# Performance work log

Measured on AMD Instinct MI355X. Metric: run time of the kernel, lower is better.

The kernel has to match this reference:

```python
import jax, jax.numpy as jnp
import numpy as np

B, T, D = 4, 2048, 1024

def setup_inputs() -> dict:
    key = jax.random.key(0)
    kx, kq, kk, kv = jax.random.split(key, 4)
    lim = 1.0 / np.sqrt(D)
    x = jax.random.normal(kx, (B, T, D), dtype=jnp.float32)
    # nn.Linear weights (stored as [out,in]); applied as x @ W.T
    W_q = jax.random.uniform(kq, (D, D), jnp.float32, -lim, lim)
    W_k = jax.random.uniform(kk, (D, D), jnp.float32, -lim, lim)
    W_v = jax.random.uniform(kv, (D, D), jnp.float32, -lim, lim)
    return {"x": x, "W_q": W_q, "W_k": W_k, "W_v": W_v}

def reference(x, W_q, W_k, W_v):
    d = x.shape[-1]
    Q = jnp.einsum('btd,ed->bte', x, W_q)
    K = jnp.einsum('btd,ed->bte', x, W_k)
    V = jnp.einsum('btd,ed->bte', x, W_v)
    att = jnp.einsum('bqd,bkd->bqk', Q, K) / jnp.sqrt(jnp.asarray(d, x.dtype))
    weights = jax.nn.softmax(att, axis=-1)  # NOTE: original applies no causal mask
    return jnp.einsum('bqk,bkd->bqd', weights, V)
```

## Files before the change

kernel.cpp:

```cpp
#include <hip/hip_runtime.h>
#include <hip/hip_bf16.h>
#include <math.h>
#include <type_traits>


typedef short shortx8 __attribute__((ext_vector_type(8)));
typedef short shortx4 __attribute__((ext_vector_type(4)));
typedef float floatx16 __attribute__((ext_vector_type(16)));
typedef __attribute__((address_space(3))) void lds_void_t;
typedef __attribute__((address_space(1))) const void gmem_void_t;

#define GLD16(gp, lp) \
    __builtin_amdgcn_global_load_lds((gmem_void_t*)(gp), (lds_void_t*)(lp), 16, 0, 0)

#define MODE_PROJ 0
#define MODE_EXP  1
#define MODE_DIV  2

template <int MODE>
__global__ __launch_bounds__(256, 2) void mfma_gemm_abt(
    const __hip_bfloat16* __restrict__ A, const __hip_bfloat16* __restrict__ B,
    void* __restrict__ Cv, float* __restrict__ rowsum,
    __hip_bfloat16* __restrict__ Vt,
    int M, int N, int K, long sA, long sB, long sC, float alpha)
{
    __shared__ __hip_bfloat16 lds[2 * 12288];

    using CT = std::conditional_t<MODE == MODE_DIV, float, __hip_bfloat16>;

    const int z = blockIdx.z;
    A += (long)z * sA;
    B += (long)z * sB;
    CT* C = (CT*)Cv + (long)z * sC;

    const int t     = threadIdx.x;
    const int wave  = t >> 6;
    const int lane  = t & 63;
    const int m0    = blockIdx.x * 256;
    const int n0    = blockIdx.y * 128;
    const int wm    = (wave >> 1) * 128;
    const int wn    = (wave & 1) * 64;
    const int lrow  = lane & 31;
    const int lhalf = lane >> 5;

    const long KU   = (long)(K >> 4);
    const long aSrc = (long)((m0 >> 5) + 2 * wave) * KU * 512 + lane * 8;
    const long bSrc = (long)((n0 >> 5) + wave) * KU * 512 + lane * 8;
    const int  dA   = wave * 2048;
    const int  dB   = 8192 + wave * 1024;

    const int raB = (wave >> 1) * 4096 + lane * 8;
    const int rbB = 8192 + (wave & 1) * 2048 + lane * 8;

#define STAGE(bo_, kt_) do {                                                  \
        _Pragma("unroll")                                                     \
        for (int q = 0; q < 2; ++q) {                                         \
            GLD16(A + aSrc + (long)(2 * (kt_) + q) * 512,                     \
                  lds + (bo_) + dA + q * 512);                                \
            GLD16(A + aSrc + (KU + 2 * (kt_) + q) * 512,                      \
                  lds + (bo_) + dA + 1024 + q * 512);                         \
            GLD16(B + bSrc + (long)(2 * (kt_) + q) * 512,                     \
                  lds + (bo_) + dB + q * 512);                                \
        }                                                                     \
    } while (0)

    floatx16 acc[4][2] = {};
    const int KT = K >> 5;

    STAGE(0, 0);
    asm volatile("s_waitcnt vmcnt(0)" ::: "memory");
    __builtin_amdgcn_s_barrier();

    for (int kt = 0; kt < KT; ++kt) {
        if (kt + 1 < KT)
            STAGE(((kt + 1) & 1) * 12288, kt + 1);

        const __hip_bfloat16* Ls = lds + (kt & 1) * 12288;

        #pragma unroll
        for (int s = 0; s < 2; ++s) {
            shortx8 a[4], b[2];
            #pragma unroll
            for (int i = 0; i < 4; ++i)
                a[i] = *(const shortx8*)(Ls + raB + i * 1024 + s * 512);
            #pragma unroll
            for (int j = 0; j < 2; ++j)
                b[j] = *(const shortx8*)(Ls + rbB + j * 1024 + s * 512);
            __builtin_amdgcn_s_setprio(1);
            #pragma unroll
            for (int i = 0; i < 4; ++i)
                #pragma unroll
                for (int j = 0; j < 2; ++j)
                    acc[i][j] = __builtin_amdgcn_mfma_f32_32x32x16_bf16(
                        a[i], b[j], acc[i][j], 0, 0, 0);
            __builtin_amdgcn_s_setprio(0);
        }
        asm volatile("s_waitcnt vmcnt(0)" ::: "memory");
        __builtin_amdgcn_s_barrier();
    }
#undef STAGE

    auto sidx = [&](int row, int col) -> long {
        return ((long)(row >> 5) * (N >> 4) + (col >> 4)) * 512
             + ((row & 31) + 32 * ((col >> 3) & 1)) * 8 + (col & 7);
    };

    if constexpr (MODE == MODE_PROJ) {
        if (z == 2) {
            const int bz   = m0 >> 11;
            const long bo2 = (long)bz * N * 2048;
            #pragma unroll
            for (int i = 0; i < 4; ++i)
                #pragma unroll
                for (int j = 0; j < 2; ++j)
                    #pragma unroll
                    for (int g = 0; g < 4; ++g) {
                        const int t0 = (m0 + wm + 32 * i + g * 8 + 4 * lhalf) & 2047;
                        const int d  = n0 + wn + 32 * j + lrow;
                        shortx4 pk;
                        #pragma unroll
                        for (int r = 0; r < 4; ++r) {
                            __hip_bfloat16 hb = __float2bfloat16(acc[i][j][4 * g + r]);
                            pk[r] = *(short*)&hb;
                        }
                        const long idx = bo2
                            + ((long)(d >> 5) * 128 + (t0 >> 4)) * 512
                            + ((d & 31) + 32 * ((t0 >> 3) & 1)) * 8 + (t0 & 7);
                        *(shortx4*)(Vt + idx) = pk;
                    }
        } else {
            #pragma unroll
            for (int i = 0; i < 4; ++i)
                #pragma unroll
                for (int j = 0; j < 2; ++j)
                    #pragma unroll
                    for (int g = 0; g < 4; ++g)
                        #pragma unroll
                        for (int r = 0; r < 4; ++r) {
                            const int row = m0 + wm + 32 * i + g * 8 + 4 * lhalf + r;
                            const int col = n0 + wn + 32 * j + lrow;
                            C[sidx(row, col)] = __float2bfloat16(acc[i][j][4 * g + r]);
                        }
        }
    } else if constexpr (MODE == MODE_EXP) {
        #pragma unroll
        for (int i = 0; i < 4; ++i) {
            float rs[16];
            #pragma unroll
            for (int reg = 0; reg < 16; ++reg) rs[reg] = 0.0f;
            #pragma unroll
            for (int j = 0; j < 2; ++j)
                #pragma unroll
                for (int g = 0; g < 4; ++g)
                    #pragma unroll
                    for (int r = 0; r < 4; ++r) {
                        const int row = m0 + wm + 32 * i + g * 8 + 4 * lhalf + r;
                        const int col = n0 + wn + 32 * j + lrow;
                        const float e = __expf(acc[i][j][4 * g + r] * alpha);
                        rs[4 * g + r] += e;
                        C[sidx(row, col)] = __float2bfloat16(e);
                    }
            #pragma unroll
            for (int reg = 0; reg < 16; ++reg) {
                float v = rs[reg];
                v += __shfl_xor(v, 1);
                v += __shfl_xor(v, 2);
                v += __shfl_xor(v, 4);
                v += __shfl_xor(v, 8);
                v += __shfl_xor(v, 16);
                if (lrow == 0) {
                    const long row = m0 + wm + 32 * i + (reg >> 2) * 8 + 4 * lhalf + (reg & 3);
                    atomicAdd(&rowsum[(long)z * M + row], v);
                }
            }
        }
    } else {
        #pragma unroll
        for (int i = 0; i < 4; ++i) {
            float inv[16];
            #pragma unroll
            for (int g = 0; g < 4; ++g)
                #pragma unroll
                for (int r = 0; r < 4; ++r) {
                    const long row = m0 + wm + 32 * i + g * 8 + 4 * lhalf + r;
                    inv[4 * g + r] = 1.0f / rowsum[(long)z * M + row];
                }
            #pragma unroll
            for (int j = 0; j < 2; ++j)
                #pragma unroll
                for (int g = 0; g < 4; ++g)
                    #pragma unroll
                    for (int r = 0; r < 4; ++r) {
                        const long row = m0 + wm + 32 * i + g * 8 + 4 * lhalf + r;
                        const long col = n0 + wn + 32 * j + lrow;
                        C[row * N + col] = acc[i][j][4 * g + r] * inv[4 * g + r];
                    }
        }
    }
}

__global__ __launch_bounds__(256) void prep(
    const float* __restrict__ x,
    const float* __restrict__ W0, const float* __restrict__ W1,
    const float* __restrict__ W2,
    __hip_bfloat16* __restrict__ xb, __hip_bfloat16* __restrict__ Wb,
    float* __restrict__ rowsum)
{
    __shared__ __hip_bfloat16 sb[32768];

    const int b  = blockIdx.x;
    const int tt = threadIdx.x;

    if (b < 32) {
        float4 zz; zz.x = zz.y = zz.z = zz.w = 0.0f;
        ((float4*)rowsum)[b * 256 + tt] = zz;
    }

    const float* src;
    __hip_bfloat16* dst;
    if (b < 256) {
        src = x + (long)b * 32 * 1024;
        dst = xb + (long)b * 32768;
    } else {
        const int w  = (b - 256) >> 5;
        const int rg = (b - 256) & 31;
        src = ((w == 0) ? W0 : (w == 1) ? W1 : W2) + (long)rg * 32 * 1024;
        dst = Wb + (long)w * 1048576 + (long)rg * 32768;
    }

    #pragma unroll
    for (int it = 0; it < 32; ++it) {
        const int idx4 = it * 256 + tt;
        const float4 f = ((const float4*)src)[idx4];
        const int row = idx4 >> 8;
        const int k0  = (idx4 & 255) << 2;
        const int p   = ((row & 31) + 32 * ((k0 >> 3) & 1)) * 8 + (k0 & 7);
        shortx4 pk;
        __hip_bfloat16 h0 = __float2bfloat16(f.x); pk[0] = *(short*)&h0;
        __hip_bfloat16 h1 = __float2bfloat16(f.y); pk[1] = *(short*)&h1;
        __hip_bfloat16 h2 = __float2bfloat16(f.z); pk[2] = *(short*)&h2;
        __hip_bfloat16 h3 = __float2bfloat16(f.w); pk[3] = *(short*)&h3;
        *(shortx4*)(sb + (k0 >> 4) * 512 + p) = pk;
    }
    __syncthreads();

    #pragma unroll
    for (int ot = 0; ot < 16; ++ot) {
        const int off = ot * 2048 + tt * 8;
        *(shortx8*)(dst + off) = *(const shortx8*)(sb + off);
    }
}

extern "C" void kernel_launch(void* const* d_in, const int* in_sizes, int n_in,
                              void* d_out, int out_size, void* d_ws, size_t ws_size,
                              hipStream_t stream)
{
    constexpr int  Bb = 4, T = 2048, D = 1024;
    constexpr int  M  = Bb * T;
    constexpr long TD = (long)T * D;
    constexpr long TT = (long)T * T;
    constexpr long MD = (long)M * D;

    const float* x  = (const float*)d_in[0];
    const float* Wq = (const float*)d_in[1];
    const float* Wk = (const float*)d_in[2];
    const float* Wv = (const float*)d_in[3];
    float* out = (float*)d_out;

    __hip_bfloat16* Q  = (__hip_bfloat16*)d_ws;
    __hip_bfloat16* Kb = Q + MD;
    __hip_bfloat16* Vt = Kb + MD;
    __hip_bfloat16* P  = Vt + MD;
    __hip_bfloat16* xb = P + (long)Bb * TT;
    __hip_bfloat16* Wb = xb + MD;
    float*     rowsum  = (float*)(Wb + 3L * D * D);

    prep<<<dim3(352), dim3(256), 0, stream>>>(x, Wq, Wk, Wv, xb, Wb, rowsum);

    dim3 blk(256);

    mfma_gemm_abt<MODE_PROJ><<<dim3(M / 256, D / 128, 3), blk, 0, stream>>>(
        xb, Wb, Q, nullptr, Vt, M, D, D, 0, (long)D * D, MD, 1.0f);

    mfma_gemm_abt<MODE_EXP><<<dim3(T / 256, T / 128, Bb), blk, 0, stream>>>(
        Q, Kb, P, rowsum, nullptr, T, T, D, TD, TD, TT, 0.03125f);

    mfma_gemm_abt<MODE_DIV><<<dim3(T / 256, D / 128, Bb), blk, 0, stream>>>(
        P, Vt, out, rowsum, nullptr, T, D, T, TT, TD, TD, 1.0f);

    (void)in_sizes; (void)n_in; (void)out_size; (void)ws_size;
}
```

Before: 249.9 us.

## Enlarge GEMM tiles to 256x256 and load B operand directly from global

Doubles the output tile per block from 256x128 to 256x256, with each wave owning a 128x128 accumulator block (4x4 MFMA tiles). The B operand is no longer staged through LDS; each wave reads its B fragments straight from global memory in the pre-swizzled layout, while only A stays double-buffered in LDS. This is meant to raise arithmetic intensity and cut LDS traffic. In exchange, register pressure doubles, which forces occupancy down to one block per CU. Global B loads are now exposed inside the loop, and the grids shrink by half, reducing the number of blocks.

```diff
diff --git a/kernel.cpp b/kernel.cpp
--- a/kernel.cpp
+++ b/kernel.cpp
@@ -18,13 +18,13 @@
 #define MODE_DIV  2
 
 template <int MODE>
-__global__ __launch_bounds__(256, 2) void mfma_gemm_abt(
+__global__ __launch_bounds__(256, 1) void mfma_gemm_abt(
     const __hip_bfloat16* __restrict__ A, const __hip_bfloat16* __restrict__ B,
     void* __restrict__ Cv, float* __restrict__ rowsum,
     __hip_bfloat16* __restrict__ Vt,
     int M, int N, int K, long sA, long sB, long sC, float alpha)
 {
-    __shared__ __hip_bfloat16 lds[2 * 12288];
+    __shared__ __hip_bfloat16 lds[2 * 8192];
 
     using CT = std::conditional_t<MODE == MODE_DIV, float, __hip_bfloat16>;
 
@@ -37,68 +37,80 @@
     const int wave  = t >> 6;
     const int lane  = t & 63;
     const int m0    = blockIdx.x * 256;
-    const int n0    = blockIdx.y * 128;
+    const int n0    = blockIdx.y * 256;
     const int wm    = (wave >> 1) * 128;
-    const int wn    = (wave & 1) * 64;
+    const int wn    = (wave & 1) * 128;
     const int lrow  = lane & 31;
     const int lhalf = lane >> 5;
 
     const long KU   = (long)(K >> 4);
     const long aSrc = (long)((m0 >> 5) + 2 * wave) * KU * 512 + lane * 8;
-    const long bSrc = (long)((n0 >> 5) + wave) * KU * 512 + lane * 8;
     const int  dA   = wave * 2048;
-    const int  dB   = 8192 + wave * 1024;
 
     const int raB = (wave >> 1) * 4096 + lane * 8;
-    const int rbB = 8192 + (wave & 1) * 2048 + lane * 8;
-
-#define STAGE(bo_, kt_) do {                                                  \
+
+    const __hip_bfloat16* pB0 =
+        B + (long)((n0 >> 5) + (wave & 1) * 4 + 0) * KU * 512 + lane * 8;
+    const __hip_bfloat16* pB1 =
+        B + (long)((n0 >> 5) + (wave & 1) * 4 + 1) * KU * 512 + lane * 8;
+    const __hip_bfloat16* pB2 =
+        B + (long)((n0 >> 5) + (wave & 1) * 4 + 2) * KU * 512 + lane * 8;
+    const __hip_bfloat16* pB3 =
+        B + (long)((n0 >> 5) + (wave & 1) * 4 + 3) * KU * 512 + lane * 8;
+
+#define STAGE_A(bo_, kt_) do {                                                \
         _Pragma("unroll")                                                     \
         for (int q = 0; q < 2; ++q) {                                         \
             GLD16(A + aSrc + (long)(2 * (kt_) + q) * 512,                     \
                   lds + (bo_) + dA + q * 512);                                \
             GLD16(A + aSrc + (KU + 2 * (kt_) + q) * 512,                      \
                   lds + (bo_) + dA + 1024 + q * 512);                         \
-            GLD16(B + bSrc + (long)(2 * (kt_) + q) * 512,                     \
-                  lds + (bo_) + dB + q * 512);                                \
         }                                                                     \
     } while (0)
 
-    floatx16 acc[4][2] = {};
+    floatx16 acc[4][4] = {};
     const int KT = K >> 5;
 
-    STAGE(0, 0);
+    STAGE_A(0, 0);
     asm volatile("s_waitcnt vmcnt(0)" ::: "memory");
     __builtin_amdgcn_s_barrier();
 
     for (int kt = 0; kt < KT; ++kt) {
+        const long kb = (long)(2 * kt) * 512;
+        shortx8 b0[4], b1[4];
+        b0[0] = *(const shortx8*)(pB0 + kb);
+        b0[1] = *(const shortx8*)(pB1 + kb);
+        b0[2] = *(const shortx8*)(pB2 + kb);
+        b0[3] = *(const shortx8*)(pB3 + kb);
+        b1[0] = *(const shortx8*)(pB0 + kb + 512);
+        b1[1] = *(const shortx8*)(pB1 + kb + 512);
+        b1[2] = *(const shortx8*)(pB2 + kb + 512);
+        b1[3] = *(const shortx8*)(pB3 + kb + 512);
+
         if (kt + 1 < KT)
-            STAGE(((kt + 1) & 1) * 12288, kt + 1);
-
-        const __hip_bfloat16* Ls = lds + (kt & 1) * 12288;
+            STAGE_A(((kt + 1) & 1) * 8192, kt + 1);
+
+        const __hip_bfloat16* Ls = lds + (kt & 1) * 8192;
 
         #pragma unroll
         for (int s = 0; s < 2; ++s) {
-            shortx8 a[4], b[2];
+            shortx8 a[4];
             #pragma unroll
             for (int i = 0; i < 4; ++i)
                 a[i] = *(const shortx8*)(Ls + raB + i * 1024 + s * 512);
-            #pragma unroll
-            for (int j = 0; j < 2; ++j)
-                b[j] = *(const shortx8*)(Ls + rbB + j * 1024 + s * 512);
             __builtin_amdgcn_s_setprio(1);
             #pragma unroll
             for (int i = 0; i < 4; ++i)
                 #pragma unroll
-                for (int j = 0; j < 2; ++j)
+                for (int j = 0; j < 4; ++j)
                     acc[i][j] = __builtin_amdgcn_mfma_f32_32x32x16_bf16(
-                        a[i], b[j], acc[i][j], 0, 0, 0);
+                        a[i], (s == 0) ? b0[j] : b1[j], acc[i][j], 0, 0, 0);
             __builtin_amdgcn_s_setprio(0);
         }
         asm volatile("s_waitcnt vmcnt(0)" ::: "memory");
         __builtin_amdgcn_s_barrier();
     }
-#undef STAGE
+#undef STAGE_A
 
     auto sidx = [&](int row, int col) -> long {
         return ((long)(row >> 5) * (N >> 4) + (col >> 4)) * 512
@@ -112,7 +124,7 @@
             #pragma unroll
             for (int i = 0; i < 4; ++i)
                 #pragma unroll
-                for (int j = 0; j < 2; ++j)
+                for (int j = 0; j < 4; ++j)
                     #pragma unroll
                     for (int g = 0; g < 4; ++g) {
                         const int t0 = (m0 + wm + 32 * i + g * 8 + 4 * lhalf) & 2047;
@@ -132,7 +144,7 @@
             #pragma unroll
             for (int i = 0; i < 4; ++i)
                 #pragma unroll
-                for (int j = 0; j < 2; ++j)
+                for (int j = 0; j < 4; ++j)
                     #pragma unroll
                     for (int g = 0; g < 4; ++g)
                         #pragma unroll
@@ -149,7 +161,7 @@
             #pragma unroll
             for (int reg = 0; reg < 16; ++reg) rs[reg] = 0.0f;
             #pragma unroll
-            for (int j = 0; j < 2; ++j)
+            for (int j = 0; j < 4; ++j)
                 #pragma unroll
                 for (int g = 0; g < 4; ++g)
                     #pragma unroll
@@ -186,7 +198,7 @@
                     inv[4 * g + r] = 1.0f / rowsum[(long)z * M + row];
                 }
             #pragma unroll
-            for (int j = 0; j < 2; ++j)
+            for (int j = 0; j < 4; ++j)
                 #pragma unroll
                 for (int g = 0; g < 4; ++g)
                     #pragma unroll
@@ -279,13 +291,13 @@
 
     dim3 blk(256);
 
-    mfma_gemm_abt<MODE_PROJ><<<dim3(M / 256, D / 128, 3), blk, 0, stream>>>(
+    mfma_gemm_abt<MODE_PROJ><<<dim3(M / 256, D / 256, 3), blk, 0, stream>>>(
         xb, Wb, Q, nullptr, Vt, M, D, D, 0, (long)D * D, MD, 1.0f);
 
-    mfma_gemm_abt<MODE_EXP><<<dim3(T / 256, T / 128, Bb), blk, 0, stream>>>(
+    mfma_gemm_abt<MODE_EXP><<<dim3(T / 256, T / 256, Bb), blk, 0, stream>>>(
         Q, Kb, P, rowsum, nullptr, T, T, D, TD, TD, TT, 0.03125f);
 
-    mfma_gemm_abt<MODE_DIV><<<dim3(T / 256, D / 128, Bb), blk, 0, stream>>>(
+    mfma_gemm_abt<MODE_DIV><<<dim3(T / 256, D / 256, Bb), blk, 0, stream>>>(
         P, Vt, out, rowsum, nullptr, T, D, T, TT, TD, TD, 1.0f);
 
     (void)in_sizes; (void)n_in; (void)out_size; (void)ws_size;
```

After: 320.2 us. 1.28x slower.
